# Kernel optimization log

Hardware: AMD Instinct MI355X
Metric: run time of the kernel (lower is better)

## Reference

```python
import jax, jax.numpy as jnp
import numpy as np
from jax import lax

B, H, L, DK = 8, 8, 1024, 64
BN_EPS = 1e-5


def _conv_bn_sm(x, w, b, g, beta, pad):
    # x: [B, H, L] (N=batch, C=h heads as channels, spatial=L)
    y = lax.conv_general_dilated(x, w, (1,), [(pad, pad)], dimension_numbers=("NCH", "OIH", "NCH"))
    y = y + b[None, :, None]
    # BatchNorm1d in training mode: batch stats over (N, L) per channel, biased var
    mu = jnp.mean(y, axis=(0, 2), keepdims=True)
    var = jnp.var(y, axis=(0, 2), keepdims=True)
    y = (y - mu) * (g[None, :, None] / jnp.sqrt(var + BN_EPS)) + beta[None, :, None]
    return jax.nn.softmax(y, axis=-1)


def setup_inputs() -> dict:
    key = jax.random.key(0)
    ks = jax.random.split(key, 20)
    n = lambda i, shape, s=1.0: jax.random.normal(ks[i], shape, dtype=jnp.float32) * s
    inp = {
        "Q": n(0, (B, H, L, DK)),
        "K": n(1, (B, H, L, DK)),
        "V": n(2, (B, H, L, DK)),
        "attn_mask": jnp.ones((1,), dtype=bool),
        # proj_q / proj_k: Linear(d_k, 1, bias=False) weight [1, d_k] -> stored as [d_k]
        "wq": n(3, (DK,), 0.1), "wk": n(4, (DK,), 0.1),
        # proj_back_q / proj_back_k: Linear(1, d_k, bias=False) weight [d_k, 1] -> [d_k]
        "wbq": n(5, (DK,), 0.1), "wbk": n(6, (DK,), 0.1),
        # Conv1d(h, h, f) weights [out=h, in=h, f] + bias [h]
        "cq3_w": n(7, (H, H, 3), 0.2), "cq3_b": n(8, (H,), 0.05),
        "cq9_w": n(9, (H, H, 9), 0.1), "cq9_b": n(10, (H,), 0.05),
        "ck3_w": n(11, (H, H, 3), 0.2), "ck3_b": n(12, (H,), 0.05),
        "ck9_w": n(13, (H, H, 9), 0.1), "ck9_b": n(14, (H,), 0.05),
        # BatchNorm1d affine params
        "bnq3_g": jnp.ones((H,), jnp.float32), "bnq3_b": jnp.zeros((H,), jnp.float32),
        "bnq9_g": jnp.ones((H,), jnp.float32), "bnq9_b": jnp.zeros((H,), jnp.float32),
        "bnk3_g": jnp.ones((H,), jnp.float32), "bnk3_b": jnp.zeros((H,), jnp.float32),
        "bnk9_g": jnp.ones((H,), jnp.float32), "bnk9_b": jnp.zeros((H,), jnp.float32),
    }
    return inp


def reference(Q, K, V, attn_mask, wq, wk, wbq, wbk,
              cq3_w, cq3_b, cq9_w, cq9_b, ck3_w, ck3_b, ck9_w, ck9_b,
              bnq3_g, bnq3_b, bnq9_g, bnq9_b, bnk3_g, bnk3_b, bnk9_g, bnk9_b):
    b, h, l, d_k = Q.shape
    l_k = K.shape[2]
    # proj to scalar per position, reshape to [b, h, l]
    Qp = jnp.einsum("bhld,d->bhl", Q, wq)
    Kp = jnp.einsum("bhld,d->bhl", K, wk)
    # multi-scale conv + BN(train) + softmax branches
    q0 = _conv_bn_sm(Qp, cq3_w, cq3_b, bnq3_g, bnq3_b, 1)
    q1 = _conv_bn_sm(Qp, cq9_w, cq9_b, bnq9_g, bnq9_b, 4)
    k0 = _conv_bn_sm(Kp, ck3_w, ck3_b, bnk3_g, bnk3_b, 1)
    k1 = _conv_bn_sm(Kp, ck9_w, ck9_b, bnk9_g, bnk9_b, 4)
    # faithful to torch: cat along dim 0 then C-order reshape to [b,h,l,2], max over last
    Qm = jnp.max(jnp.concatenate([q0, q1], axis=0).reshape(b, h, l, 2), axis=-1)
    Km = jnp.max(jnp.concatenate([k0, k1], axis=0).reshape(b, h, l_k, 2), axis=-1)
    # proj back 1 -> d_k (no bias): outer with weight vector
    Qn = Qm[..., None] * wbq  # [b,h,l,d_k]
    Kn = Km[..., None] * wbk  # [b,h,l_k,d_k]
    scores = jnp.einsum("bhqd,bhkd->bhqk", Qn, Kn) / jnp.sqrt(jnp.float32(d_k))
    attn = jax.nn.softmax(scores, axis=-1)
    context = jnp.einsum("bhqk,bhkd->bhqd", attn, V)
    return (context, attn)
```

## Files before the change

### kernel.cpp

```cpp
#include <hip/hip_runtime.h>

constexpr int SL = 1024;
constexpr int NBH = 64;

constexpr int QP_OFF = 0;
constexpr int KP_OFF = 65536;
constexpr int Y_OFF  = 131072;
constexpr int QM_OFF = 655360;
constexpr int KM_OFF = 720896;
constexpr int ST_OFF = 786432;
constexpr int C_OFF  = 786496;
constexpr int VT_OFF = 786560;

typedef __attribute__((ext_vector_type(8))) short short8;
typedef __attribute__((ext_vector_type(4))) float f32x4;

__device__ inline unsigned short f2bf(float x) {
    unsigned int u = __float_as_uint(x);
    unsigned int r = (u + 0x7fff + ((u >> 16) & 1)) >> 16;
    return (unsigned short)r;
}

__global__ __launch_bounds__(256) void k_projpack(
    const float* __restrict__ Q, const float* __restrict__ K,
    const float* __restrict__ V,
    const float* __restrict__ wq, const float* __restrict__ wk,
    const float* __restrict__ wbq, const float* __restrict__ wbk,
    float* __restrict__ ws)
{
    int b = blockIdx.x;
    int tid = threadIdx.x;
    if (b < 8192) {
        bool isQ = b < 4096;
        const float* src = isQ ? Q : K;
        const float* w   = isQ ? wq : wk;
        int row = (b - (isQ ? 0 : 4096)) * 16 + (tid >> 4);
        int l16 = tid & 15;
        float4 x  = ((const float4*)(src + row * 64))[l16];
        float4 w4 = ((const float4*)w)[l16];
        float v = x.x * w4.x + x.y * w4.y + x.z * w4.z + x.w * w4.w;
        #pragma unroll
        for (int m = 8; m; m >>= 1) v += __shfl_xor(v, m);
        if (l16 == 0) ws[(isQ ? QP_OFF : KP_OFF) + row] = v;
    } else if (b < 10240) {
        int t = (b - 8192) * 256 + tid;
        int lane = t & 63;
        int s    = (t >> 6) & 7;
        int dsub = (t >> 9) & 3;
        int chunk= (t >> 11) & 3;
        int bh   = t >> 13;
        const float* vb = V + bh * (SL * 64);
        int k0 = chunk * 256 + s * 32 + (lane >> 4) * 8;
        int d  = dsub * 16 + (lane & 15);
        unsigned short o[8];
        #pragma unroll
        for (int j = 0; j < 8; j++) o[j] = f2bf(vb[(k0 + j) * 64 + d]);
        unsigned short* vt = (unsigned short*)(ws + VT_OFF);
        *(short8*)(vt + (size_t)t * 8) = *(short8*)o;
    } else {
        if (tid < 64) {
            ws[ST_OFF + tid] = 0.f;
            float v = wbq[tid] * wbk[tid];
            #pragma unroll
            for (int m = 32; m; m >>= 1) v += __shfl_xor(v, m);
            if (tid == 0) ws[C_OFF] = v * 0.125f;
        }
    }
}

__global__ __launch_bounds__(256) void k_conv(
    float* __restrict__ ws,
    const float* __restrict__ w0, const float* __restrict__ b0,
    const float* __restrict__ w1, const float* __restrict__ b1,
    const float* __restrict__ w2, const float* __restrict__ b2,
    const float* __restrict__ w3, const float* __restrict__ b3)
{
    int branch = blockIdx.x >> 6;
    int n = (blockIdx.x >> 3) & 7;
    int seg = blockIdx.x & 7;
    int t0 = seg * 128;
    const float* wp = branch == 0 ? w0 : branch == 1 ? w1 : branch == 2 ? w2 : w3;
    const float* bp = branch == 0 ? b0 : branch == 1 ? b1 : branch == 2 ? b2 : b3;
    const int F = (branch & 1) ? 9 : 3;
    const int PAD = F >> 1;
    const float* x = ws + ((branch < 2) ? QP_OFF : KP_OFF) + n * 8 * SL;

    __shared__ float xl[8][136];
    __shared__ float wl[8 * 8 * 9];
    __shared__ float bl[8];
    int tid = threadIdx.x;
    for (int i = tid; i < 8 * 8 * F; i += 256) wl[i] = wp[i];
    if (tid < 8) bl[tid] = bp[tid];
    for (int i = tid; i < 8 * 136; i += 256) {
        int ci = i / 136; int tt = i - ci * 136;
        int ta = t0 + tt - 4;
        xl[ci][tt] = (ta >= 0 && ta < SL) ? x[ci * SL + ta] : 0.f;
    }
    __syncthreads();
    int c = tid >> 5, u = tid & 31;
    float s1 = 0.f, s2 = 0.f;
    float* yout = ws + Y_OFF + branch * (NBH * SL) + (n * 8 + c) * SL + t0;
    #pragma unroll
    for (int q = 0; q < 4; q++) {
        int tl = q * 32 + u;
        float acc = bl[c];
        for (int ci = 0; ci < 8; ci++) {
            const float* xr = &xl[ci][tl + 4 - PAD];
            const float* wr = &wl[(c * 8 + ci) * F];
            for (int f = 0; f < F; f++) acc += wr[f] * xr[f];
        }
        yout[tl] = acc;
        s1 += acc; s2 += acc * acc;
    }
    #pragma unroll
    for (int m = 16; m; m >>= 1) {
        s1 += __shfl_xor(s1, m);
        s2 += __shfl_xor(s2, m);
    }
    if (u == 0) {
        atomicAdd(&ws[ST_OFF + (branch * 8 + c) * 2],     s1);
        atomicAdd(&ws[ST_OFF + (branch * 8 + c) * 2 + 1], s2);
    }
}

__global__ __launch_bounds__(256) void k_bnmix(
    float* __restrict__ ws,
    const float* __restrict__ g0, const float* __restrict__ be0,
    const float* __restrict__ g1, const float* __restrict__ be1,
    const float* __restrict__ g2, const float* __restrict__ be2,
    const float* __restrict__ g3, const float* __restrict__ be3)
{
    int blk = blockIdx.x;
    int which = blk >> 6;
    int i = (blk >> 3) & 7, j = blk & 7;
    int n = 2 * i + (j >= 4 ? 1 : 0);
    int br = which * 2 + (n >= 8 ? 1 : 0);
    int row = n & 7;
    int tid = threadIdx.x;
    int half = tid >> 7;
    int u = tid & 127;
    int c = 2 * (j & 3) + half;
    const float* gp = br == 0 ? g0 : br == 1 ? g1 : br == 2 ? g2 : g3;
    const float* bp = br == 0 ? be0 : br == 1 ? be1 : br == 2 ? be2 : be3;
    float s1 = ws[ST_OFF + (br * 8 + c) * 2];
    float s2 = ws[ST_OFF + (br * 8 + c) * 2 + 1];
    float mu  = s1 * (1.f / 8192.f);
    float var = s2 * (1.f / 8192.f) - mu * mu;
    float sc = gp[c] * rsqrtf(var + 1e-5f);
    float sh = bp[c] - mu * sc;
    const float* y = ws + Y_OFF + br * (NBH * SL) + (row * 8 + c) * SL;
    float4 ya = ((const float4*)y)[u * 2];
    float4 yb = ((const float4*)y)[u * 2 + 1];
    float z[8] = { ya.x * sc + sh, ya.y * sc + sh, ya.z * sc + sh, ya.w * sc + sh,
                   yb.x * sc + sh, yb.y * sc + sh, yb.z * sc + sh, yb.w * sc + sh };
    float mx = z[0];
    #pragma unroll
    for (int q = 1; q < 8; q++) mx = fmaxf(mx, z[q]);
    __shared__ float r1[4], r2[4];
    #pragma unroll
    for (int m = 32; m; m >>= 1) mx = fmaxf(mx, __shfl_xor(mx, m));
    if ((tid & 63) == 0) r1[tid >> 6] = mx;
    __syncthreads();
    mx = half ? fmaxf(r1[2], r1[3]) : fmaxf(r1[0], r1[1]);
    float e[8];
    float s = 0.f;
    #pragma unroll
    for (int q = 0; q < 8; q++) { e[q] = __expf(z[q] - mx); s += e[q]; }
    #pragma unroll
    for (int m = 32; m; m >>= 1) s += __shfl_xor(s, m);
    if ((tid & 63) == 0) r2[tid >> 6] = s;
    __syncthreads();
    s = half ? (r2[2] + r2[3]) : (r2[0] + r2[1]);
    float inv = 1.f / s;
    float4 o = make_float4(fmaxf(e[0], e[1]) * inv, fmaxf(e[2], e[3]) * inv,
                           fmaxf(e[4], e[5]) * inv, fmaxf(e[6], e[7]) * inv);
    float* outp = ws + (which ? KM_OFF : QM_OFF) + i * 8192 + j * 1024 + half * 512;
    ((float4*)outp)[u] = o;
}

__global__ __launch_bounds__(256) void k_attn(
    float* __restrict__ out, const float* __restrict__ ws)
{
    int p = blockIdx.x;
    int xcd = p & 7, jj = p >> 3;
    int bh = xcd + 8 * (jj >> 4);
    int qt = jj & 15;
    int tid = threadIdx.x;
    __shared__ float kml[1024];
    __shared__ float aq[64], mq[64], rq[64];
    __shared__ float red[256];
    __shared__ float rmx[4], rmn[4];

    const float* km = ws + KM_OFF + bh * SL;
    const float* qm = ws + QM_OFF + bh * SL + qt * 64;
    float c = ws[C_OFF];

    float lmax = -1e30f, lmin = 1e30f;
    #pragma unroll
    for (int i = 0; i < 4; i++) {
        float v = km[tid + 256 * i];
        kml[tid + 256 * i] = v;
        lmax = fmaxf(lmax, v); lmin = fminf(lmin, v);
    }
    #pragma unroll
    for (int m = 32; m; m >>= 1) {
        lmax = fmaxf(lmax, __shfl_xor(lmax, m));
        lmin = fminf(lmin, __shfl_xor(lmin, m));
    }
    if ((tid & 63) == 0) { rmx[tid >> 6] = lmax; rmn[tid >> 6] = lmin; }
    __syncthreads();
    float kmax = fmaxf(fmaxf(rmx[0], rmx[1]), fmaxf(rmx[2], rmx[3]));
    float kmin = fminf(fminf(rmn[0], rmn[1]), fminf(rmn[2], rmn[3]));
    if (tid < 64) {
        float a = c * qm[tid];
        aq[tid] = a;
        mq[tid] = (a > 0.f) ? a * kmax : a * kmin;
    }
    __syncthreads();
    {
        int q = tid >> 2, g = tid & 3;
        float a = aq[q], m = mq[q];
        float s = 0.f;
        const float4* kp4 = ((const float4*)kml) + g * 64;
        for (int k = 0; k < 64; k++) {
            float4 kv = kp4[k];
            s += __expf(a * kv.x - m) + __expf(a * kv.y - m)
               + __expf(a * kv.z - m) + __expf(a * kv.w - m);
        }
        red[tid] = s;
        __syncthreads();
        if (tid < 64) {
            float d = red[tid * 4] + red[tid * 4 + 1] + red[tid * 4 + 2] + red[tid * 4 + 3];
            rq[tid] = 1.f / d;
        }
        __syncthreads();
    }

    int w = tid >> 6, lane = tid & 63;
    int m16 = lane & 15, kg = lane >> 4;
    int qloc = w * 16 + m16;
    float a = aq[qloc], mm = mq[qloc], rr = rq[qloc];
    float* attn_row = out + 4194304 + ((size_t)(bh * SL + qt * 64 + qloc)) * SL;
    const short8* vt8 = (const short8*)((const unsigned short*)(ws + VT_OFF))
                        + (size_t)bh * 8192;

    f32x4 acc0 = {0,0,0,0}, acc1 = {0,0,0,0}, acc2 = {0,0,0,0}, acc3 = {0,0,0,0};

    for (int ch = 0; ch < 4; ch++) {
        const short8* vch = vt8 + ch * 2048;
        #pragma unroll
        for (int s = 0; s < 8; s++) {
            int k0 = ch * 256 + s * 32 + kg * 8;
            const float4* kp = (const float4*)(kml + k0);
            float4 ka = kp[0], kb = kp[1];
            float e[8];
            e[0] = __expf(a * ka.x - mm) * rr;
            e[1] = __expf(a * ka.y - mm) * rr;
            e[2] = __expf(a * ka.z - mm) * rr;
            e[3] = __expf(a * ka.w - mm) * rr;
            e[4] = __expf(a * kb.x - mm) * rr;
            e[5] = __expf(a * kb.y - mm) * rr;
            e[6] = __expf(a * kb.z - mm) * rr;
            e[7] = __expf(a * kb.w - mm) * rr;
            *(float4*)(attn_row + k0)     = make_float4(e[0], e[1], e[2], e[3]);
            *(float4*)(attn_row + k0 + 4) = make_float4(e[4], e[5], e[6], e[7]);
            unsigned short af[8];
            #pragma unroll
            for (int j = 0; j < 8; j++) af[j] = f2bf(e[j]);
            short8 av = *(short8*)af;
            const short8* bbase = vch + s * 64 + lane;
            short8 b0 = bbase[0 * 512];
            short8 b1 = bbase[1 * 512];
            short8 b2 = bbase[2 * 512];
            short8 b3 = bbase[3 * 512];
            acc0 = __builtin_amdgcn_mfma_f32_16x16x32_bf16(av, b0, acc0, 0, 0, 0);
            acc1 = __builtin_amdgcn_mfma_f32_16x16x32_bf16(av, b1, acc1, 0, 0, 0);
            acc2 = __builtin_amdgcn_mfma_f32_16x16x32_bf16(av, b2, acc2, 0, 0, 0);
            acc3 = __builtin_amdgcn_mfma_f32_16x16x32_bf16(av, b3, acc3, 0, 0, 0);
        }
    }
    float* ctx = out + ((size_t)(bh * SL + qt * 64 + w * 16)) * 64;
    #pragma unroll
    for (int reg = 0; reg < 4; reg++) {
        int row = kg * 4 + reg;
        float* cp = ctx + row * 64 + m16;
        cp[0]  = acc0[reg];
        cp[16] = acc1[reg];
        cp[32] = acc2[reg];
        cp[48] = acc3[reg];
    }
}

extern "C" void kernel_launch(void* const* d_in, const int* in_sizes, int n_in,
                              void* d_out, int out_size, void* d_ws, size_t ws_size,
                              hipStream_t stream)
{
    const float* Q      = (const float*)d_in[0];
    const float* K      = (const float*)d_in[1];
    const float* V      = (const float*)d_in[2];
    const float* wq     = (const float*)d_in[4];
    const float* wk     = (const float*)d_in[5];
    const float* wbq    = (const float*)d_in[6];
    const float* wbk    = (const float*)d_in[7];
    const float* cq3_w  = (const float*)d_in[8];
    const float* cq3_b  = (const float*)d_in[9];
    const float* cq9_w  = (const float*)d_in[10];
    const float* cq9_b  = (const float*)d_in[11];
    const float* ck3_w  = (const float*)d_in[12];
    const float* ck3_b  = (const float*)d_in[13];
    const float* ck9_w  = (const float*)d_in[14];
    const float* ck9_b  = (const float*)d_in[15];
    const float* bnq3_g = (const float*)d_in[16];
    const float* bnq3_b = (const float*)d_in[17];
    const float* bnq9_g = (const float*)d_in[18];
    const float* bnq9_b = (const float*)d_in[19];
    const float* bnk3_g = (const float*)d_in[20];
    const float* bnk3_b = (const float*)d_in[21];
    const float* bnk9_g = (const float*)d_in[22];
    const float* bnk9_b = (const float*)d_in[23];
    float* out = (float*)d_out;
    float* ws  = (float*)d_ws;

    k_projpack<<<10241, 256, 0, stream>>>(Q, K, V, wq, wk, wbq, wbk, ws);
    k_conv<<<256, 256, 0, stream>>>(ws, cq3_w, cq3_b, cq9_w, cq9_b,
                                    ck3_w, ck3_b, ck9_w, ck9_b);
    k_bnmix<<<128, 256, 0, stream>>>(ws, bnq3_g, bnq3_b, bnq9_g, bnq9_b,
                                     bnk3_g, bnk3_b, bnk9_g, bnk9_b);
    k_attn<<<1024, 256, 0, stream>>>(out, ws);
}
```

Before: 412.7 us.

## Split attention key range across waves and keep exponentials in registers

```diff
diff --git a/kernel.cpp b/kernel.cpp
--- a/kernel.cpp
+++ b/kernel.cpp
@@ -178,21 +178,23 @@
     ((float4*)outp)[u] = o;
 }
 
-__global__ __launch_bounds__(256) void k_attn(
+__global__ __launch_bounds__(256, 4) void k_attn(
     float* __restrict__ out, const float* __restrict__ ws)
 {
     int p = blockIdx.x;
-    int xcd = p & 7, jj = p >> 3;
-    int bh = xcd + 8 * (jj >> 4);
-    int qt = jj & 15;
+    int xcd = p & 7, idx = p >> 3;
+    int bh = xcd + 8 * (idx >> 6);
+    int qt = idx & 63;
     int tid = threadIdx.x;
-    __shared__ float kml[1024];
-    __shared__ float aq[64], mq[64], rq[64];
-    __shared__ float red[256];
+
+    __shared__ __align__(16) float kml[1024];
+    __shared__ float aql[16], mql[16];
     __shared__ float rmx[4], rmn[4];
+    __shared__ float wsum[4][16];
+    __shared__ float accred[4][16][64];
 
     const float* km = ws + KM_OFF + bh * SL;
-    const float* qm = ws + QM_OFF + bh * SL + qt * 64;
+    const float* qm = ws + QM_OFF + bh * SL + qt * 16;
     float c = ws[C_OFF];
 
     float lmax = -1e30f, lmin = 1e30f;
@@ -209,85 +211,93 @@
     }
     if ((tid & 63) == 0) { rmx[tid >> 6] = lmax; rmn[tid >> 6] = lmin; }
     __syncthreads();
-    float kmax = fmaxf(fmaxf(rmx[0], rmx[1]), fmaxf(rmx[2], rmx[3]));
-    float kmin = fminf(fminf(rmn[0], rmn[1]), fminf(rmn[2], rmn[3]));
-    if (tid < 64) {
+    if (tid < 16) {
+        float kmax = fmaxf(fmaxf(rmx[0], rmx[1]), fmaxf(rmx[2], rmx[3]));
+        float kmin = fminf(fminf(rmn[0], rmn[1]), fminf(rmn[2], rmn[3]));
         float a = c * qm[tid];
-        aq[tid] = a;
-        mq[tid] = (a > 0.f) ? a * kmax : a * kmin;
-    }
-    __syncthreads();
-    {
-        int q = tid >> 2, g = tid & 3;
-        float a = aq[q], m = mq[q];
-        float s = 0.f;
-        const float4* kp4 = ((const float4*)kml) + g * 64;
-        for (int k = 0; k < 64; k++) {
-            float4 kv = kp4[k];
-            s += __expf(a * kv.x - m) + __expf(a * kv.y - m)
-               + __expf(a * kv.z - m) + __expf(a * kv.w - m);
-        }
-        red[tid] = s;
-        __syncthreads();
-        if (tid < 64) {
-            float d = red[tid * 4] + red[tid * 4 + 1] + red[tid * 4 + 2] + red[tid * 4 + 3];
-            rq[tid] = 1.f / d;
-        }
-        __syncthreads();
-    }
+        aql[tid] = a;
+        mql[tid] = (a > 0.f) ? a * kmax : a * kmin;
+    }
+    __syncthreads();
 
     int w = tid >> 6, lane = tid & 63;
     int m16 = lane & 15, kg = lane >> 4;
-    int qloc = w * 16 + m16;
-    float a = aq[qloc], mm = mq[qloc], rr = rq[qloc];
-    float* attn_row = out + 4194304 + ((size_t)(bh * SL + qt * 64 + qloc)) * SL;
+    float a = aql[m16], mm = mql[m16];
+
+    float e[64];
+    float rowsum = 0.f;
+    #pragma unroll
+    for (int s = 0; s < 8; s++) {
+        const float4* kp = (const float4*)(kml + w * 256 + s * 32 + kg * 8);
+        float4 ka = kp[0], kb = kp[1];
+        e[s * 8 + 0] = __expf(a * ka.x - mm);
+        e[s * 8 + 1] = __expf(a * ka.y - mm);
+        e[s * 8 + 2] = __expf(a * ka.z - mm);
+        e[s * 8 + 3] = __expf(a * ka.w - mm);
+        e[s * 8 + 4] = __expf(a * kb.x - mm);
+        e[s * 8 + 5] = __expf(a * kb.y - mm);
+        e[s * 8 + 6] = __expf(a * kb.z - mm);
+        e[s * 8 + 7] = __expf(a * kb.w - mm);
+        #pragma unroll
+        for (int j = 0; j < 8; j++) rowsum += e[s * 8 + j];
+    }
+    rowsum += __shfl_xor(rowsum, 16);
+    rowsum += __shfl_xor(rowsum, 32);
+    if (lane < 16) wsum[w][lane] = rowsum;
+    __syncthreads();
+    float rr = 1.f / (wsum[0][m16] + wsum[1][m16] + wsum[2][m16] + wsum[3][m16]);
+
+    float* attn_row = out + 4194304 + ((size_t)(bh * SL + qt * 16 + m16)) * SL;
     const short8* vt8 = (const short8*)((const unsigned short*)(ws + VT_OFF))
-                        + (size_t)bh * 8192;
+                        + (size_t)bh * 8192 + w * 2048;
 
     f32x4 acc0 = {0,0,0,0}, acc1 = {0,0,0,0}, acc2 = {0,0,0,0}, acc3 = {0,0,0,0};
 
-    for (int ch = 0; ch < 4; ch++) {
-        const short8* vch = vt8 + ch * 2048;
-        #pragma unroll
-        for (int s = 0; s < 8; s++) {
-            int k0 = ch * 256 + s * 32 + kg * 8;
-            const float4* kp = (const float4*)(kml + k0);
-            float4 ka = kp[0], kb = kp[1];
-            float e[8];
-            e[0] = __expf(a * ka.x - mm) * rr;
-            e[1] = __expf(a * ka.y - mm) * rr;
-            e[2] = __expf(a * ka.z - mm) * rr;
-            e[3] = __expf(a * ka.w - mm) * rr;
-            e[4] = __expf(a * kb.x - mm) * rr;
-            e[5] = __expf(a * kb.y - mm) * rr;
-            e[6] = __expf(a * kb.z - mm) * rr;
-            e[7] = __expf(a * kb.w - mm) * rr;
-            *(float4*)(attn_row + k0)     = make_float4(e[0], e[1], e[2], e[3]);
-            *(float4*)(attn_row + k0 + 4) = make_float4(e[4], e[5], e[6], e[7]);
-            unsigned short af[8];
-            #pragma unroll
-            for (int j = 0; j < 8; j++) af[j] = f2bf(e[j]);
-            short8 av = *(short8*)af;
-            const short8* bbase = vch + s * 64 + lane;
-            short8 b0 = bbase[0 * 512];
-            short8 b1 = bbase[1 * 512];
-            short8 b2 = bbase[2 * 512];
-            short8 b3 = bbase[3 * 512];
-            acc0 = __builtin_amdgcn_mfma_f32_16x16x32_bf16(av, b0, acc0, 0, 0, 0);
-            acc1 = __builtin_amdgcn_mfma_f32_16x16x32_bf16(av, b1, acc1, 0, 0, 0);
-            acc2 = __builtin_amdgcn_mfma_f32_16x16x32_bf16(av, b2, acc2, 0, 0, 0);
-            acc3 = __builtin_amdgcn_mfma_f32_16x16x32_bf16(av, b3, acc3, 0, 0, 0);
-        }
-    }
-    float* ctx = out + ((size_t)(bh * SL + qt * 64 + w * 16)) * 64;
+    #pragma unroll
+    for (int s = 0; s < 8; s++) {
+        int k0 = w * 256 + s * 32 + kg * 8;
+        float es[8];
+        #pragma unroll
+        for (int j = 0; j < 8; j++) es[j] = e[s * 8 + j] * rr;
+        *(float4*)(attn_row + k0)     = make_float4(es[0], es[1], es[2], es[3]);
+        *(float4*)(attn_row + k0 + 4) = make_float4(es[4], es[5], es[6], es[7]);
+        unsigned short af[8];
+        #pragma unroll
+        for (int j = 0; j < 8; j++) af[j] = f2bf(es[j]);
+        short8 av = *(short8*)af;
+        const short8* bbase = vt8 + s * 64 + lane;
+        short8 b0 = bbase[0 * 512];
+        short8 b1 = bbase[1 * 512];
+        short8 b2 = bbase[2 * 512];
+        short8 b3 = bbase[3 * 512];
+        acc0 = __builtin_amdgcn_mfma_f32_16x16x32_bf16(av, b0, acc0, 0, 0, 0);
+        acc1 = __builtin_amdgcn_mfma_f32_16x16x32_bf16(av, b1, acc1, 0, 0, 0);
+        acc2 = __builtin_amdgcn_mfma_f32_16x16x32_bf16(av, b2, acc2, 0, 0, 0);
+        acc3 = __builtin_amdgcn_mfma_f32_16x16x32_bf16(av, b3, acc3, 0, 0, 0);
+    }
+
     #pragma unroll
     for (int reg = 0; reg < 4; reg++) {
-        int row = kg * 4 + reg;
-        float* cp = ctx + row * 64 + m16;
-        cp[0]  = acc0[reg];
-        cp[16] = acc1[reg];
-        cp[32] = acc2[reg];
-        cp[48] = acc3[reg];
+        int r = kg * 4 + reg;
+        accred[w][r][ 0 + m16] = acc0[reg];
+        accred[w][r][16 + m16] = acc1[reg];
+        accred[w][r][32 + m16] = acc2[reg];
+        accred[w][r][48 + m16] = acc3[reg];
+    }
+    __syncthreads();
+    {
+        int r  = tid >> 4;
+        int d0 = (tid & 15) * 4;
+        float4 s0 = *(const float4*)&accred[0][r][d0];
+        float4 s1 = *(const float4*)&accred[1][r][d0];
+        float4 s2 = *(const float4*)&accred[2][r][d0];
+        float4 s3 = *(const float4*)&accred[3][r][d0];
+        float4 o = make_float4(s0.x + s1.x + s2.x + s3.x,
+                               s0.y + s1.y + s2.y + s3.y,
+                               s0.z + s1.z + s2.z + s3.z,
+                               s0.w + s1.w + s2.w + s3.w);
+        float* ctx = out + ((size_t)(bh * SL + qt * 16 + r)) * 64 + d0;
+        *(float4*)ctx = o;
     }
 }
 
@@ -326,5 +336,5 @@
                                     ck3_w, ck3_b, ck9_w, ck9_b);
     k_bnmix<<<128, 256, 0, stream>>>(ws, bnq3_g, bnq3_b, bnq9_g, bnq9_b,
                                      bnk3_g, bnk3_b, bnk9_g, bnk9_b);
-    k_attn<<<1024, 256, 0, stream>>>(out, ws);
-}
+    k_attn<<<4096, 256, 0, stream>>>(out, ws);
+}
```

Measured after the change: 394.4 us. 1.05x faster.
